# Optimization experiments

Hardware: AMD Instinct MI355X
Metric: run time of the kernel (lower is better)

The kernel has to match this reference:

```python
import jax, jax.numpy as jnp
import numpy as np

N, E, B = 20000, 320000, 64
HID, DEPTH, NFREQ = 128, 4, 8
NODE_DIM, EDGE_DIM, SG = 4, 3, 230
TWO_PI = 2.0 * np.pi


def setup_inputs() -> dict:
    key = jax.random.key(0)
    ks = jax.random.split(key, 20)
    inp = {}
    inp["x"] = jax.random.normal(ks[0], (N, NODE_DIM), jnp.float32)
    inp["edge_index"] = jax.random.randint(ks[1], (2, E), 0, N)
    inp["edge_attr"] = jax.random.normal(ks[2], (E, EDGE_DIM), jnp.float32)
    inp["batch"] = jnp.sort(jax.random.randint(ks[3], (N,), 0, B))
    inp["space_group"] = jax.random.randint(ks[4], (B,), 0, SG)
    inp["node_w"] = jax.random.normal(ks[5], (NODE_DIM, HID), jnp.float32) * 0.1
    inp["node_b"] = jnp.zeros((HID,), jnp.float32)
    inp["sg_table"] = jax.random.normal(ks[6], (SG, HID), jnp.float32) * 0.1
    inp["lin_w"] = jax.random.normal(ks[7], (DEPTH, 2 * HID + EDGE_DIM, HID), jnp.float32) * 0.05
    inp["lin_b"] = jnp.zeros((DEPTH, HID), jnp.float32)
    inp["att_w"] = jax.random.normal(ks[8], (DEPTH, 2 * HID + EDGE_DIM), jnp.float32) * 0.05
    inp["att_b"] = jnp.zeros((DEPTH,), jnp.float32)
    inp["fk_w"] = jax.random.normal(ks[9], (DEPTH, NFREQ, HID, HID), jnp.float32) * 0.1
    inp["fk_b"] = jnp.zeros((DEPTH, HID), jnp.float32)
    inp["bn_g"] = jnp.ones((DEPTH, HID), jnp.float32)
    inp["bn_b"] = jnp.zeros((DEPTH, HID), jnp.float32)
    inp["pool_w"] = jax.random.normal(ks[10], (HID,), jnp.float32) * 0.1
    inp["pool_b"] = jnp.zeros((), jnp.float32)
    inp["head_w1"] = jax.random.normal(ks[11], (4, 2 * HID, HID), jnp.float32) * 0.05
    inp["head_b1"] = jnp.zeros((4, HID), jnp.float32)
    for i, (nm, od) in enumerate([("e", 1), ("s", 3), ("c", 7), ("m", 3)]):
        inp[nm + "_w2"] = jax.random.normal(ks[12 + i], (HID, od), jnp.float32) * 0.05
        inp[nm + "_b2"] = jnp.zeros((od,), jnp.float32)
    return inp


def reference(x, edge_index, edge_attr, batch, space_group, node_w, node_b, sg_table,
              lin_w, lin_b, att_w, att_b, fk_w, fk_b, bn_g, bn_b, pool_w, pool_b,
              head_w1, head_b1, e_w2, e_b2, s_w2, s_b2, c_w2, c_b2, m_w2, m_b2):
    src, dst = edge_index[0], edge_index[1]  # x_j = x[src], x_i = x[dst]
    h = x @ node_w + node_b                  # [N, HID]
    sg = sg_table[space_group]               # [B, HID]
    freqs = jnp.arange(1, NFREQ + 1, dtype=h.dtype)
    for l in range(DEPTH):
        # edge conv: gather-concat-linear-sigmoid attention-scatter add
        tmp = jnp.concatenate([h[dst], h[src], edge_attr], axis=-1)   # [E, 2H+3]
        alpha = jax.nn.sigmoid(tmp @ att_w[l] + att_b[l])[:, None]    # [E, 1]
        msg = alpha * (tmp @ lin_w[l] + lin_b[l])                     # [E, H]
        h_conv = jax.ops.segment_sum(msg, dst, num_segments=N)
        # Fourier-Kolmogorov branch
        ang = TWO_PI * freqs[None, :, None] * h[:, None, :]           # [N, K, H]
        h_fk = (jnp.einsum('nki,kio->no', jnp.sin(ang), fk_w[l])
                + jnp.einsum('nki,kio->no', jnp.cos(ang), fk_w[l]) + fk_b[l])
        h = h_conv + h_fk
        # BatchNorm1d (batch statistics, training semantics) + ReLU; dropout = identity (eval)
        mu = h.mean(axis=0)
        var = h.var(axis=0)
        h = (h - mu) / jnp.sqrt(var + 1e-5) * bn_g[l] + bn_b[l]
        h = jax.nn.relu(h)
    # attention pool: softmax over ALL nodes (dim=0), as in the original
    a = jax.nn.softmax(h @ pool_w + pool_b, axis=0)[:, None]          # [N, 1]
    pooled = jax.ops.segment_sum(a * h, batch, num_segments=B)        # [B, H]
    comb = jnp.concatenate([pooled, sg], axis=-1)                     # [B, 2H]

    def head(i, w2, b2):
        z = jax.nn.relu(comb @ head_w1[i] + head_b1[i])
        return z @ w2 + b2

    energy = head(0, e_w2, e_b2)          # [B, 1]
    stability = head(1, s_w2, s_b2)       # [B, 3]
    crystal_system = head(2, c_w2, c_b2)  # [B, 7]
    material_type = head(3, m_w2, m_b2)   # [B, 3]
    return energy, stability, crystal_system, material_type
```

## Files before the change

kernel.cpp:

```cpp
#include <hip/hip_runtime.h>
#include <math.h>

#define HID 128
#define DEPTH 4
#define PSPLIT 16
#define SMAXB 40

typedef _Float16 half8 __attribute__((ext_vector_type(8)));
typedef float f4 __attribute__((ext_vector_type(4)));

__global__ void k_node_embed(const float* __restrict__ x, const float* __restrict__ nw,
                             const float* __restrict__ nb, float* __restrict__ h, int N) {
    int idx = blockIdx.x * blockDim.x + threadIdx.x;
    if (idx >= N * HID) return;
    int n = idx >> 7, c = idx & 127;
    float acc = nb[c];
#pragma unroll
    for (int d = 0; d < 4; ++d) acc += x[n * 4 + d] * nw[d * HID + c];
    h[idx] = acc;
}

__global__ void k_wsplit(const float* __restrict__ fkw, _Float16* __restrict__ whi,
                         _Float16* __restrict__ wlo) {
    __shared__ float sh[64][65];
    int bid = blockIdx.x;
    int l = bid >> 5; int r = bid & 31; int kb = r >> 1; int nbk = r & 1;
    const float* W = fkw + (size_t)l * 131072;
    _Float16* Hl = whi + (size_t)l * 131072;
    _Float16* Ll = wlo + (size_t)l * 131072;
    int k0 = kb * 64, n0 = nbk * 64;
    for (int i = threadIdx.x; i < 4096; i += 256) {
        int kk = i >> 6, nn = i & 63;
        sh[kk][nn] = W[(k0 + kk) * HID + n0 + nn];
    }
    __syncthreads();
    for (int i = threadIdx.x; i < 4096; i += 256) {
        int nn = i >> 6, kk = i & 63;
        float w = sh[kk][nn];
        _Float16 hi = (_Float16)w;
        _Float16 lo = (_Float16)((w - (float)hi) * 2048.f);
        Hl[(n0 + nn) * 1024 + k0 + kk] = hi;
        Ll[(n0 + nn) * 1024 + k0 + kk] = lo;
    }
}

__global__ void k_wsplit2(const float* __restrict__ linw, _Float16* __restrict__ lwhi,
                          _Float16* __restrict__ lwlo) {
    __shared__ float sh[64][65];
    int bid = blockIdx.x;
    int l = bid >> 3; int r = bid & 7; int cb = r >> 1; int kb = r & 1;
    const float* W = linw + (size_t)l * 259 * HID;
    int c0 = cb * 64, k0 = kb * 64;
    const float* base = W + (size_t)((c0 >= 128) ? 128 : 0) * HID + (c0 & 127);
    for (int i = threadIdx.x; i < 4096; i += 256) {
        int kk = i >> 6, cc = i & 63;
        sh[kk][cc] = base[(size_t)(k0 + kk) * HID + cc];
    }
    __syncthreads();
    _Float16* Hl = lwhi + (size_t)l * 32768;
    _Float16* Ll = lwlo + (size_t)l * 32768;
    for (int i = threadIdx.x; i < 4096; i += 256) {
        int cc = i >> 6, kk = i & 63;
        float w = sh[kk][cc];
        _Float16 hi = (_Float16)w;
        _Float16 lo = (_Float16)((w - (float)hi) * 2048.f);
        Hl[(size_t)(c0 + cc) * 128 + k0 + kk] = hi;
        Ll[(size_t)(c0 + cc) * 128 + k0 + kk] = lo;
    }
}

__global__ void k_hist(const int* __restrict__ dst, int* __restrict__ deg, int E) {
    int e = blockIdx.x * 256 + threadIdx.x;
    if (e < E) atomicAdd(&deg[dst[e]], 1);
}

__global__ void k_scan_a(const int* __restrict__ deg, int* __restrict__ bsum, int N) {
    __shared__ int sh[256];
    int i = blockIdx.x * 256 + threadIdx.x;
    sh[threadIdx.x] = (i < N) ? deg[i] : 0;
    __syncthreads();
    for (int off = 128; off > 0; off >>= 1) {
        if (threadIdx.x < (unsigned)off) sh[threadIdx.x] += sh[threadIdx.x + off];
        __syncthreads();
    }
    if (threadIdx.x == 0) bsum[blockIdx.x] = sh[0];
}

__global__ void k_scan_b(int* __restrict__ bsum, int nb) {
    __shared__ int sh[256];
    int v = (threadIdx.x < (unsigned)nb) ? bsum[threadIdx.x] : 0;
    sh[threadIdx.x] = v;
    __syncthreads();
    for (int off = 1; off < 256; off <<= 1) {
        int add = (threadIdx.x >= (unsigned)off) ? sh[threadIdx.x - off] : 0;
        __syncthreads();
        sh[threadIdx.x] += add;
        __syncthreads();
    }
    if (threadIdx.x < (unsigned)nb) bsum[threadIdx.x] = sh[threadIdx.x] - v;
}

__global__ void k_scan_c(const int* __restrict__ deg, const int* __restrict__ bsum,
                         int* __restrict__ offs, int* __restrict__ cursor, int N) {
    __shared__ int sh[256];
    int i = blockIdx.x * 256 + threadIdx.x;
    int v = (i < N) ? deg[i] : 0;
    sh[threadIdx.x] = v;
    __syncthreads();
    for (int off = 1; off < 256; off <<= 1) {
        int add = (threadIdx.x >= (unsigned)off) ? sh[threadIdx.x - off] : 0;
        __syncthreads();
        sh[threadIdx.x] += add;
        __syncthreads();
    }
    int ex = bsum[blockIdx.x] + sh[threadIdx.x] - v;
    if (i < N) { offs[i] = ex; cursor[i] = ex; }
    if (i == N - 1) offs[N] = ex + v;
}

__global__ void k_scatter(const int* __restrict__ src, const int* __restrict__ dst,
                          const float* __restrict__ ea, int* cursor,
                          int* __restrict__ srco, float4* __restrict__ ea3o, int E) {
    int e = blockIdx.x * 256 + threadIdx.x;
    if (e < E) {
        int d = dst[e];
        int p = atomicAdd(&cursor[d], 1);
        srco[p] = src[e];
        float4 q;
        q.x = ea[e * 3 + 0]; q.y = ea[e * 3 + 1]; q.z = ea[e * 3 + 2]; q.w = 0.f;
        ea3o[p] = q;
    }
}

__global__ void k_bstart(const int* __restrict__ batch, int* __restrict__ boffs, int N, int B) {
    int n = blockIdx.x * 256 + threadIdx.x;
    if (n >= N) return;
    int b1 = batch[n];
    if (n == 0) for (int b = 0; b <= b1; ++b) boffs[b] = 0;
    int b2 = (n + 1 < N) ? batch[n + 1] : B;
    for (int b = b1 + 1; b <= b2; ++b) boffs[b] = n + 1;
}

__global__ __launch_bounds__(512, 4) void k_nlgemm(const float* __restrict__ h,
        const _Float16* __restrict__ lwhi, const _Float16* __restrict__ lwlo,
        const float* __restrict__ linb,
        const float* __restrict__ attw, const float* __restrict__ attb,
        float* __restrict__ A1, float* __restrict__ A2,
        float* __restrict__ a1, float* __restrict__ a2, int N) {
    __shared__ _Float16 ahi[32 * 128];
    __shared__ _Float16 alo[32 * 128];
    int tid = threadIdx.x;
    int nb = blockIdx.x * 32;
    {
        int row = tid >> 4;
        int o16 = tid & 15;
        int gn = nb + row;
        int rc = (gn < N) ? gn : (N - 1);
        const float* hp = h + (size_t)rc * HID + o16 * 8;
        float hv[8];
        *(float4*)&hv[0] = *(const float4*)hp;
        *(float4*)&hv[4] = *(const float4*)(hp + 4);
        float p1 = 0.f, p2 = 0.f;
#pragma unroll
        for (int j = 0; j < 8; ++j) {
            int k = o16 * 8 + j;
            p1 += hv[j] * attw[k];
            p2 += hv[j] * attw[128 + k];
        }
        for (int off = 8; off > 0; off >>= 1) {
            p1 += __shfl_down(p1, off, 16);
            p2 += __shfl_down(p2, off, 16);
        }
        if (o16 == 0 && gn < N) {
            a1[gn] = p1 + attb[0];
            a2[gn] = p2;
        }
        int rs = row & 7;
        half8 vh, vl;
#pragma unroll
        for (int j = 0; j < 8; ++j) {
            float a = hv[j];
            _Float16 hi = (_Float16)a;
            vh[j] = hi;
            vl[j] = (_Float16)((a - (float)hi) * 2048.f);
        }
        int oct = o16 ^ rs;
        *(half8*)&ahi[row * 128 + oct * 8] = vh;
        *(half8*)&alo[row * 128 + oct * 8] = vl;
    }
    __syncthreads();
    int lane = tid & 63, wv = tid >> 6;
    int quad = lane >> 4, l16 = lane & 15;
    int n0 = wv * 32;
    f4 acc0[2][2], accL[2][2];
#pragma unroll
    for (int mi = 0; mi < 2; ++mi)
#pragma unroll
        for (int ni = 0; ni < 2; ++ni) { acc0[mi][ni] = (f4)(0.f); accL[mi][ni] = (f4)(0.f); }
    const _Float16* bhp0 = lwhi + (size_t)(n0 + l16) * 128 + quad * 8;
    const _Float16* bhp1 = lwhi + (size_t)(n0 + 16 + l16) * 128 + quad * 8;
    const _Float16* blp0 = lwlo + (size_t)(n0 + l16) * 128 + quad * 8;
    const _Float16* blp1 = lwlo + (size_t)(n0 + 16 + l16) * 128 + quad * 8;
    int rs16 = (l16 & 7) << 3;
#pragma unroll
    for (int step = 0; step < 4; ++step) {
        int ka = (step * 32 + quad * 8) ^ rs16;
        int ko = step * 32;
        half8 bh0 = *(const half8*)(bhp0 + ko);
        half8 bh1 = *(const half8*)(bhp1 + ko);
        half8 bl0 = *(const half8*)(blp0 + ko);
        half8 bl1 = *(const half8*)(blp1 + ko);
        half8 ah[2], al[2];
#pragma unroll
        for (int mi = 0; mi < 2; ++mi) {
            ah[mi] = *(const half8*)&ahi[(l16 + mi * 16) * 128 + ka];
            al[mi] = *(const half8*)&alo[(l16 + mi * 16) * 128 + ka];
        }
#pragma unroll
        for (int mi = 0; mi < 2; ++mi) {
            acc0[mi][0] = __builtin_amdgcn_mfma_f32_16x16x32_f16(ah[mi], bh0, acc0[mi][0], 0, 0, 0);
            acc0[mi][1] = __builtin_amdgcn_mfma_f32_16x16x32_f16(ah[mi], bh1, acc0[mi][1], 0, 0, 0);
            accL[mi][0] = __builtin_amdgcn_mfma_f32_16x16x32_f16(ah[mi], bl0, accL[mi][0], 0, 0, 0);
            accL[mi][1] = __builtin_amdgcn_mfma_f32_16x16x32_f16(ah[mi], bl1, accL[mi][1], 0, 0, 0);
            accL[mi][0] = __builtin_amdgcn_mfma_f32_16x16x32_f16(al[mi], bh0, accL[mi][0], 0, 0, 0);
            accL[mi][1] = __builtin_amdgcn_mfma_f32_16x16x32_f16(al[mi], bh1, accL[mi][1], 0, 0, 0);
        }
    }
    const float inv = 1.0f / 2048.0f;
#pragma unroll
    for (int mi = 0; mi < 2; ++mi)
#pragma unroll
        for (int ni = 0; ni < 2; ++ni)
#pragma unroll
            for (int r = 0; r < 4; ++r) {
                int gn = nb + mi * 16 + quad * 4 + r;
                if (gn >= N) continue;
                int cp = n0 + ni * 16 + l16;
                float val = acc0[mi][ni][r] + accL[mi][ni][r] * inv;
                if (cp < 128) A1[(size_t)gn * HID + cp] = val + linb[cp];
                else          A2[(size_t)gn * HID + cp - 128] = val;
            }
}

__global__ __launch_bounds__(256) void k_edge(const float* __restrict__ A1,
        const float* __restrict__ A2, const float* __restrict__ a1,
        const float* __restrict__ a2, const int* __restrict__ srco,
        const float4* __restrict__ ea3o, const int* __restrict__ offs,
        const float* __restrict__ linw3, const float* __restrict__ attw3,
        float* __restrict__ hconv, double* __restrict__ stats, int N) {
    __shared__ float part[8][HID + 4];
    int n = blockIdx.x;
    int tid = threadIdx.x;
    if (n == 0) stats[tid] = 0.0;
    int lane32 = tid & 31, slot = tid >> 5;
    int c4 = lane32 * 4;
    float4 w0v = *(const float4*)&linw3[c4];
    float4 w1v = *(const float4*)&linw3[HID + c4];
    float4 w2v = *(const float4*)&linw3[2 * HID + c4];
    float aw0 = attw3[0], aw1 = attw3[1], aw2 = attw3[2];
    float a1n = a1[n];
    float4 A1v = *(const float4*)&A1[(size_t)n * HID + c4];
    float4 acc; acc.x = acc.y = acc.z = acc.w = 0.f;
    int s0 = offs[n], s1 = offs[n + 1];
    for (int idx = s0 + slot; idx < s1; idx += 8) {
        int s = srco[idx];
        float4 q = ea3o[idx];
        float logit = a1n + a2[s] + q.x * aw0 + q.y * aw1 + q.z * aw2;
        float al = 1.f / (1.f + __expf(-logit));
        float4 a2v = *(const float4*)&A2[(size_t)s * HID + c4];
        float4 pre;
        pre.x = A1v.x + a2v.x + q.x * w0v.x + q.y * w1v.x + q.z * w2v.x;
        pre.y = A1v.y + a2v.y + q.x * w0v.y + q.y * w1v.y + q.z * w2v.y;
        pre.z = A1v.z + a2v.z + q.x * w0v.z + q.y * w1v.z + q.z * w2v.z;
        pre.w = A1v.w + a2v.w + q.x * w0v.w + q.y * w1v.w + q.z * w2v.w;
        acc.x += al * pre.x; acc.y += al * pre.y;
        acc.z += al * pre.z; acc.w += al * pre.w;
    }
    *(float4*)&part[slot][c4] = acc;
    __syncthreads();
    if (slot == 0) {
        float4 p = *(const float4*)&part[0][c4];
#pragma unroll
        for (int s = 1; s < 8; ++s) {
            float4 r = *(const float4*)&part[s][c4];
            p.x += r.x; p.y += r.y; p.z += r.z; p.w += r.w;
        }
        *(float4*)&hconv[(size_t)n * HID + c4] = p;
    }
}

#define FK_MT 64
__global__ __launch_bounds__(512, 4) void k_fk(const float* __restrict__ h,
        const _Float16* __restrict__ whi, const _Float16* __restrict__ wlo,
        float* __restrict__ p0, float* __restrict__ p1,
        float* __restrict__ p2, float* __restrict__ p3, int N) {
    __shared__ _Float16 ahi[FK_MT * 256];
    __shared__ _Float16 alo[FK_MT * 256];
    int tid = threadIdx.x;
    int bx = blockIdx.x;
    int nb = (bx >> 2) * FK_MT;
    int ks = bx & 3;
    int kbase = ks * 256;
    int fr0 = kbase >> 7;
    {
        int row = tid >> 3;
        int o8 = tid & 7;
        int gn = nb + row;
        int rc = (gn < N) ? gn : (N - 1);
        const float* hp = h + (size_t)rc * HID + o8 * 8;
        float hv[2][8];
        *(float4*)&hv[0][0] = *(const float4*)hp;
        *(float4*)&hv[0][4] = *(const float4*)(hp + 4);
        *(float4*)&hv[1][0] = *(const float4*)(hp + 64);
        *(float4*)&hv[1][4] = *(const float4*)(hp + 68);
        int rs = row & 7;
#pragma unroll
        for (int g = 0; g < 2; ++g) {
            float freqf = 6.2831853f * (float)(fr0 + g + 1);
#pragma unroll
            for (int s = 0; s < 2; ++s) {
                half8 vh, vl;
#pragma unroll
                for (int j = 0; j < 8; ++j) {
                    float ang = freqf * hv[s][j] + 0.78539816f;
                    float a = 1.41421356f * __sinf(ang);
                    _Float16 hi = (_Float16)a;
                    vh[j] = hi;
                    vl[j] = (_Float16)((a - (float)hi) * 2048.f);
                }
                int oct = (g * 16 + s * 8 + o8) ^ rs;
                *(half8*)&ahi[row * 256 + oct * 8] = vh;
                *(half8*)&alo[row * 256 + oct * 8] = vl;
            }
        }
    }
    __syncthreads();
    int lane = tid & 63, wv = tid >> 6;
    int quad = lane >> 4, l16 = lane & 15;
    int n0w = wv * 16;
    f4 acc0[4], accL[4];
#pragma unroll
    for (int mi = 0; mi < 4; ++mi) { acc0[mi] = (f4)(0.f); accL[mi] = (f4)(0.f); }
    const _Float16* bhp = whi + (size_t)(n0w + l16) * 1024 + kbase + quad * 8;
    const _Float16* blp = wlo + (size_t)(n0w + l16) * 1024 + kbase + quad * 8;
    int rs16 = (l16 & 7) << 3;
#pragma unroll 2
    for (int step = 0; step < 8; ++step) {
        int ka = (step * 32 + quad * 8) ^ rs16;
        int ko = step * 32;
        half8 bh = *(const half8*)(bhp + ko);
        half8 bl = *(const half8*)(blp + ko);
        half8 ah[4], al[4];
#pragma unroll
        for (int mi = 0; mi < 4; ++mi) {
            ah[mi] = *(const half8*)&ahi[(l16 + mi * 16) * 256 + ka];
            al[mi] = *(const half8*)&alo[(l16 + mi * 16) * 256 + ka];
        }
#pragma unroll
        for (int mi = 0; mi < 4; ++mi) {
            acc0[mi] = __builtin_amdgcn_mfma_f32_16x16x32_f16(ah[mi], bh, acc0[mi], 0, 0, 0);
            accL[mi] = __builtin_amdgcn_mfma_f32_16x16x32_f16(ah[mi], bl, accL[mi], 0, 0, 0);
            accL[mi] = __builtin_amdgcn_mfma_f32_16x16x32_f16(al[mi], bh, accL[mi], 0, 0, 0);
        }
    }
    float* p = (ks == 0) ? p0 : (ks == 1) ? p1 : (ks == 2) ? p2 : p3;
    const float inv = 1.0f / 2048.0f;
#pragma unroll
    for (int mi = 0; mi < 4; ++mi)
#pragma unroll
        for (int r = 0; r < 4; ++r) {
            int gn = nb + mi * 16 + quad * 4 + r;
            if (gn < N)
                p[gn * HID + n0w + l16] = acc0[mi][r] + accL[mi][r] * inv;
        }
}

__global__ __launch_bounds__(256) void k_bn_stats(float* __restrict__ hconv,
                           const float* __restrict__ p0, const float* __restrict__ p1,
                           const float* __restrict__ p2, const float* __restrict__ p3,
                           const float* __restrict__ fkb,
                           double* __restrict__ stats, int N) {
    int tid = threadIdx.x;
    int cq = tid & 31, rg = tid >> 5;
    int c4 = cq * 4;
    float4 bias = *(const float4*)&fkb[c4];
    float s1[4] = {0, 0, 0, 0}, s2[4] = {0, 0, 0, 0};
    for (int n = blockIdx.x * 8 + rg; n < N; n += gridDim.x * 8) {
        size_t idx = (size_t)n * HID + c4;
        float4 a  = *(const float4*)&hconv[idx];
        float4 b0 = *(const float4*)&p0[idx];
        float4 b1 = *(const float4*)&p1[idx];
        float4 b2 = *(const float4*)&p2[idx];
        float4 b3 = *(const float4*)&p3[idx];
        float4 v;
        v.x = a.x + b0.x + b1.x + b2.x + b3.x + bias.x;
        v.y = a.y + b0.y + b1.y + b2.y + b3.y + bias.y;
        v.z = a.z + b0.z + b1.z + b2.z + b3.z + bias.z;
        v.w = a.w + b0.w + b1.w + b2.w + b3.w + bias.w;
        *(float4*)&hconv[idx] = v;
        s1[0] += v.x; s2[0] += v.x * v.x;
        s1[1] += v.y; s2[1] += v.y * v.y;
        s1[2] += v.z; s2[2] += v.z * v.z;
        s1[3] += v.w; s2[3] += v.w * v.w;
    }
#pragma unroll
    for (int j = 0; j < 4; ++j) {
        s1[j] += __shfl_down(s1[j], 32);
        s2[j] += __shfl_down(s2[j], 32);
    }
    __shared__ float sh1[4][32][4], sh2[4][32][4];
    int wv = tid >> 6, lane = tid & 63;
    if (lane < 32) {
#pragma unroll
        for (int j = 0; j < 4; ++j) { sh1[wv][lane][j] = s1[j]; sh2[wv][lane][j] = s2[j]; }
    }
    __syncthreads();
    if (tid < 128) {
        int cq2 = tid >> 2, j2 = tid & 3;
        float t1 = sh1[0][cq2][j2] + sh1[1][cq2][j2] + sh1[2][cq2][j2] + sh1[3][cq2][j2];
        float t2 = sh2[0][cq2][j2] + sh2[1][cq2][j2] + sh2[2][cq2][j2] + sh2[3][cq2][j2];
        int c = cq2 * 4 + j2;
        atomicAdd(&stats[c], (double)t1);
        atomicAdd(&stats[128 + c], (double)t2);
    }
}

__global__ void k_bn_apply(const float* __restrict__ hsum, const double* __restrict__ stats,
                           const float* __restrict__ g, const float* __restrict__ b,
                           const float* __restrict__ pw, const float* __restrict__ pb,
                           float* __restrict__ h, float* __restrict__ s,
                           int do_score, int N) {
    int idx = blockIdx.x * 256 + threadIdx.x;
    int row = idx >> 5, cq = idx & 31;
    int c4 = cq * 4;
    int valid = row < N;
    double invN = 1.0 / (double)N;
    float p = 0.f;
    if (valid) {
        float4 hv = *(const float4*)&hsum[(size_t)row * HID + c4];
        float vin[4] = {hv.x, hv.y, hv.z, hv.w};
        float4 ov;
        float* po = &ov.x;
#pragma unroll
        for (int j = 0; j < 4; ++j) {
            int c = c4 + j;
            float mu = (float)(stats[c] * invN);
            float var = (float)(stats[128 + c] * invN) - mu * mu;
            float inv = 1.f / sqrtf(var + 1e-5f);
            float sc = g[c] * inv;
            float sh = b[c] - mu * sc;
            float oo = fmaxf(vin[j] * sc + sh, 0.f);
            po[j] = oo;
            if (do_score) p += oo * pw[c];
        }
        *(float4*)&h[(size_t)row * HID + c4] = ov;
    }
    if (do_score) {
        for (int off = 16; off > 0; off >>= 1) p += __shfl_down(p, off, 32);
        if ((threadIdx.x & 31) == 0 && valid) s[row] = p + pb[0];
    }
}

__global__ void k_smax1(const float* __restrict__ s, float* __restrict__ mzp, int N) {
    __shared__ float red[256];
    float m = -INFINITY;
    for (int n = blockIdx.x * 256 + threadIdx.x; n < N; n += SMAXB * 256)
        m = fmaxf(m, s[n]);
    red[threadIdx.x] = m;
    __syncthreads();
    for (int off = 128; off > 0; off >>= 1) {
        if (threadIdx.x < (unsigned)off)
            red[threadIdx.x] = fmaxf(red[threadIdx.x], red[threadIdx.x + off]);
        __syncthreads();
    }
    m = red[0];
    __syncthreads();
    float z = 0.f;
    for (int n = blockIdx.x * 256 + threadIdx.x; n < N; n += SMAXB * 256)
        z += __expf(s[n] - m);
    red[threadIdx.x] = z;
    __syncthreads();
    for (int off = 128; off > 0; off >>= 1) {
        if (threadIdx.x < (unsigned)off) red[threadIdx.x] += red[threadIdx.x + off];
        __syncthreads();
    }
    if (threadIdx.x == 0) { mzp[blockIdx.x * 2] = m; mzp[blockIdx.x * 2 + 1] = red[0]; }
}

__device__ __forceinline__ void combine_mz(const float* mzp, float& m, float& Z) {
    m = -INFINITY;
#pragma unroll 8
    for (int i = 0; i < SMAXB; ++i) m = fmaxf(m, mzp[i * 2]);
    Z = 0.f;
#pragma unroll 8
    for (int i = 0; i < SMAXB; ++i) Z += mzp[i * 2 + 1] * __expf(mzp[i * 2] - m);
}

__global__ void k_pool_part(const float* __restrict__ h, const float* __restrict__ s,
                            const float* __restrict__ mzp, const int* __restrict__ boffs,
                            float* __restrict__ part) {
    int b = blockIdx.x >> 4, split = blockIdx.x & (PSPLIT - 1);
    int c = threadIdx.x & 127, half = threadIdx.x >> 7;
    float m, Z;
    combine_mz(mzp, m, Z);
    (void)Z;
    int n0 = boffs[b], n1 = boffs[b + 1];
    float acc = 0.f;
    for (int n = n0 + split * 2 + half; n < n1; n += PSPLIT * 2)
        acc += __expf(s[n] - m) * h[n * HID + c];
    __shared__ float prt[2][HID];
    prt[half][c] = acc;
    __syncthreads();
    if (half == 0) part[(size_t)(b * PSPLIT + split) * HID + c] = prt[0][c] + prt[1][c];
}

__global__ void k_pool_sum(const float* __restrict__ part, const float* __restrict__ mzp,
                           float* __restrict__ pooled) {
    int b = blockIdx.x, c = threadIdx.x;
    float m, Z;
    combine_mz(mzp, m, Z);
    float acc = 0.f;
#pragma unroll
    for (int i = 0; i < PSPLIT; ++i) acc += part[(size_t)(b * PSPLIT + i) * HID + c];
    pooled[b * HID + c] = acc / Z;
}

__global__ __launch_bounds__(256) void k_head(const float* __restrict__ pooled,
                       const float* __restrict__ sg_table,
                       const int* __restrict__ space_group,
                       const float* __restrict__ hw1, const float* __restrict__ hb1,
                       const float* __restrict__ ew2, const float* __restrict__ eb2,
                       const float* __restrict__ sw2, const float* __restrict__ sb2,
                       const float* __restrict__ cw2, const float* __restrict__ cb2,
                       const float* __restrict__ mw2, const float* __restrict__ mb2,
                       float* __restrict__ out, int B) {
    __shared__ float comb[256];
    __shared__ float zred[2][128];
    __shared__ float zsh[128];
    int b = blockIdx.x >> 2, i = blockIdx.x & 3;
    int t = threadIdx.x;
    comb[t] = (t < 128) ? pooled[b * HID + t] : sg_table[space_group[b] * HID + (t - 128)];
    __syncthreads();
    int half = t >> 7, tt = t & 127;
    const float* W = hw1 + ((size_t)i * 256 + half * 128) * HID;
    const float* cb = &comb[half * 128];
    float z = 0.f;
#pragma unroll 8
    for (int k = 0; k < 128; ++k) z += cb[k] * W[k * HID + tt];
    zred[half][tt] = z;
    __syncthreads();
    if (t < 128) zsh[t] = fmaxf(zred[0][t] + zred[1][t] + hb1[i * HID + t], 0.f);
    __syncthreads();
    const int od[4] = {1, 3, 7, 3};
    const int base[4] = {0, 64, 256, 704};
    const float* w2 = (i == 0) ? ew2 : (i == 1) ? sw2 : (i == 2) ? cw2 : mw2;
    const float* b2 = (i == 0) ? eb2 : (i == 1) ? sb2 : (i == 2) ? cb2 : mb2;
    int odi = od[i];
    if (t < odi) {
        float o = b2[t];
        for (int c = 0; c < HID; ++c) o += zsh[c] * w2[c * odi + t];
        out[base[i] + b * odi + t] = o;
    }
}

extern "C" void kernel_launch(void* const* d_in, const int* in_sizes, int n_in,
                              void* d_out, int out_size, void* d_ws, size_t ws_size,
                              hipStream_t stream) {
    const float* x          = (const float*)d_in[0];
    const int*   edge_index = (const int*)d_in[1];
    const float* edge_attr  = (const float*)d_in[2];
    const int*   batch      = (const int*)d_in[3];
    const int*   space_group= (const int*)d_in[4];
    const float* node_w     = (const float*)d_in[5];
    const float* node_b     = (const float*)d_in[6];
    const float* sg_table   = (const float*)d_in[7];
    const float* lin_w      = (const float*)d_in[8];
    const float* lin_b      = (const float*)d_in[9];
    const float* att_w      = (const float*)d_in[10];
    const float* att_b      = (const float*)d_in[11];
    const float* fk_w       = (const float*)d_in[12];
    const float* fk_b       = (const float*)d_in[13];
    const float* bn_g       = (const float*)d_in[14];
    const float* bn_b       = (const float*)d_in[15];
    const float* pool_w     = (const float*)d_in[16];
    const float* pool_b     = (const float*)d_in[17];
    const float* head_w1    = (const float*)d_in[18];
    const float* head_b1    = (const float*)d_in[19];
    const float* ew2 = (const float*)d_in[20]; const float* eb2 = (const float*)d_in[21];
    const float* sw2 = (const float*)d_in[22]; const float* sb2 = (const float*)d_in[23];
    const float* cw2 = (const float*)d_in[24]; const float* cb2 = (const float*)d_in[25];
    const float* mw2 = (const float*)d_in[26]; const float* mb2 = (const float*)d_in[27];
    float* out = (float*)d_out;

    const int N = in_sizes[3];
    const int E = in_sizes[1] / 2;
    const int B = in_sizes[4];
    const int* src = edge_index;
    const int* dst = edge_index + E;

    char* w = (char*)d_ws;
    auto alloc = [&](size_t bytes) { char* p = w; w += (bytes + 255) & ~(size_t)255; return p; };
    float*  h      = (float*)alloc((size_t)N * HID * 4);
    float*  A1     = (float*)alloc((size_t)N * HID * 4);
    float*  A2     = (float*)alloc((size_t)N * HID * 4);
    float*  p2     = (float*)alloc((size_t)N * HID * 4);
    float*  p3     = (float*)alloc((size_t)N * HID * 4);
    float*  hconv  = (float*)alloc((size_t)N * HID * 4);
    float*  a1     = (float*)alloc((size_t)N * 4);
    float*  a2     = (float*)alloc((size_t)N * 4);
    float*  sbuf   = (float*)alloc((size_t)N * 4);
    int*    deg    = (int*)alloc((size_t)N * 4);
    int*    cursor = (int*)alloc((size_t)N * 4);
    int*    offs   = (int*)alloc((size_t)(N + 1) * 4);
    int*    srco   = (int*)alloc((size_t)E * 4);
    float4* ea3o   = (float4*)alloc((size_t)E * 16);
    _Float16* whi  = (_Float16*)alloc((size_t)DEPTH * 1024 * HID * 2);
    _Float16* wlo  = (_Float16*)alloc((size_t)DEPTH * 1024 * HID * 2);
    _Float16* lwhi = (_Float16*)alloc((size_t)DEPTH * 256 * HID * 2);
    _Float16* lwlo = (_Float16*)alloc((size_t)DEPTH * 256 * HID * 2);
    int*    bsum   = (int*)alloc(256 * 4);
    int*    boffs  = (int*)alloc((size_t)(B + 1) * 4);
    double* stats  = (double*)alloc(256 * 8);
    float*  mzp    = (float*)alloc(SMAXB * 2 * 4);
    float*  part   = (float*)alloc((size_t)B * PSPLIT * HID * 4);
    float*  pooled = (float*)alloc((size_t)B * HID * 4);

    const int nchunk = (N + 255) / 256;
    const int echunk = (E + 255) / 256;

    k_wsplit<<<128, 256, 0, stream>>>(fk_w, whi, wlo);
    k_wsplit2<<<32, 256, 0, stream>>>(lin_w, lwhi, lwlo);
    hipMemsetAsync(deg, 0, (size_t)N * 4, stream);
    k_hist<<<echunk, 256, 0, stream>>>(dst, deg, E);
    k_scan_a<<<nchunk, 256, 0, stream>>>(deg, bsum, N);
    k_scan_b<<<1, 256, 0, stream>>>(bsum, nchunk);
    k_scan_c<<<nchunk, 256, 0, stream>>>(deg, bsum, offs, cursor, N);
    k_scatter<<<echunk, 256, 0, stream>>>(src, dst, edge_attr, cursor, srco, ea3o, E);
    k_bstart<<<nchunk, 256, 0, stream>>>(batch, boffs, N, B);

    k_node_embed<<<(N * HID + 255) / 256, 256, 0, stream>>>(x, node_w, node_b, h, N);

    for (int l = 0; l < DEPTH; ++l) {
        const float* linw_l = lin_w + (size_t)l * 259 * HID;
        k_nlgemm<<<(N + 31) / 32, 512, 0, stream>>>(
            h, lwhi + (size_t)l * 32768, lwlo + (size_t)l * 32768,
            lin_b + l * HID, att_w + (size_t)l * 259, att_b + l,
            A1, A2, a1, a2, N);
        k_edge<<<N, 256, 0, stream>>>(A1, A2, a1, a2, srco, ea3o, offs,
                                      linw_l + 256 * HID, att_w + (size_t)l * 259 + 256,
                                      hconv, stats, N);
        k_fk<<<((N + FK_MT - 1) / FK_MT) * 4, 512, 0, stream>>>(
            h, whi + (size_t)l * 131072, wlo + (size_t)l * 131072, A1, A2, p2, p3, N);
        k_bn_stats<<<320, 256, 0, stream>>>(hconv, A1, A2, p2, p3, fk_b + l * HID, stats, N);
        k_bn_apply<<<(N * 32 + 255) / 256, 256, 0, stream>>>(
            hconv, stats, bn_g + l * HID, bn_b + l * HID, pool_w, pool_b,
            h, sbuf, (l == DEPTH - 1) ? 1 : 0, N);
    }

    k_smax1<<<SMAXB, 256, 0, stream>>>(sbuf, mzp, N);
    k_pool_part<<<B * PSPLIT, 256, 0, stream>>>(h, sbuf, mzp, boffs, part);
    k_pool_sum<<<B, 128, 0, stream>>>(part, mzp, pooled);
    k_head<<<B * 4, 256, 0, stream>>>(pooled, sg_table, space_group, head_w1, head_b1,
                                      ew2, eb2, sw2, sb2, cw2, cb2, mw2, mb2, out, B);
}
```

Baseline: 645.8 us.

## Fuse node embedding and BatchNorm apply into next layer's GEMM prologues

Removes the standalone node-embed kernel and the per-layer BN-apply kernel. The first layer's GEMM and Fourier kernels now compute the embedding from x directly, and later layers apply the previous layer's BatchNorm and ReLU while loading their input. Per-layer stats buffers are zeroed once up front, and hconv is double-buffered so the raw pre-BN activations survive until both consumers have read them. This saves one full N x HID write and read pass per layer plus launches, at the cost of recomputing the BN scale and shift in every thread of two kernels.

```diff
diff --git a/kernel.cpp b/kernel.cpp
--- a/kernel.cpp
+++ b/kernel.cpp
@@ -8,17 +8,6 @@
 
 typedef _Float16 half8 __attribute__((ext_vector_type(8)));
 typedef float f4 __attribute__((ext_vector_type(4)));
-
-__global__ void k_node_embed(const float* __restrict__ x, const float* __restrict__ nw,
-                             const float* __restrict__ nb, float* __restrict__ h, int N) {
-    int idx = blockIdx.x * blockDim.x + threadIdx.x;
-    if (idx >= N * HID) return;
-    int n = idx >> 7, c = idx & 127;
-    float acc = nb[c];
-#pragma unroll
-    for (int d = 0; d < 4; ++d) acc += x[n * 4 + d] * nw[d * HID + c];
-    h[idx] = acc;
-}
 
 __global__ void k_wsplit(const float* __restrict__ fkw, _Float16* __restrict__ whi,
                          _Float16* __restrict__ wlo) {
@@ -141,7 +130,10 @@
     for (int b = b1 + 1; b <= b2; ++b) boffs[b] = n + 1;
 }
 
-__global__ __launch_bounds__(512, 4) void k_nlgemm(const float* __restrict__ h,
+__global__ __launch_bounds__(512, 4) void k_nlgemm(const float* __restrict__ hsrc,
+        const float* __restrict__ x, const float* __restrict__ nw, const float* __restrict__ nbv,
+        const double* __restrict__ bnst, const float* __restrict__ bng, const float* __restrict__ bnb,
+        int mode,
         const _Float16* __restrict__ lwhi, const _Float16* __restrict__ lwlo,
         const float* __restrict__ linb,
         const float* __restrict__ attw, const float* __restrict__ attb,
@@ -156,10 +148,31 @@
         int o16 = tid & 15;
         int gn = nb + row;
         int rc = (gn < N) ? gn : (N - 1);
-        const float* hp = h + (size_t)rc * HID + o16 * 8;
         float hv[8];
-        *(float4*)&hv[0] = *(const float4*)hp;
-        *(float4*)&hv[4] = *(const float4*)(hp + 4);
+        if (mode == 0) {
+            float4 xr = *(const float4*)&x[(size_t)rc * 4];
+#pragma unroll
+            for (int j = 0; j < 8; ++j) {
+                int c = o16 * 8 + j;
+                hv[j] = nbv[c] + xr.x * nw[c] + xr.y * nw[HID + c]
+                       + xr.z * nw[2 * HID + c] + xr.w * nw[3 * HID + c];
+            }
+        } else {
+            const float* hp = hsrc + (size_t)rc * HID + o16 * 8;
+            *(float4*)&hv[0] = *(const float4*)hp;
+            *(float4*)&hv[4] = *(const float4*)(hp + 4);
+            double invN = 1.0 / (double)N;
+#pragma unroll
+            for (int j = 0; j < 8; ++j) {
+                int c = o16 * 8 + j;
+                float mu = (float)(bnst[c] * invN);
+                float var = (float)(bnst[128 + c] * invN) - mu * mu;
+                float inv = 1.f / sqrtf(var + 1e-5f);
+                float sc = bng[c] * inv;
+                float sh = bnb[c] - mu * sc;
+                hv[j] = fmaxf(hv[j] * sc + sh, 0.f);
+            }
+        }
         float p1 = 0.f, p2 = 0.f;
 #pragma unroll
         for (int j = 0; j < 8; ++j) {
@@ -247,11 +260,10 @@
         const float* __restrict__ a2, const int* __restrict__ srco,
         const float4* __restrict__ ea3o, const int* __restrict__ offs,
         const float* __restrict__ linw3, const float* __restrict__ attw3,
-        float* __restrict__ hconv, double* __restrict__ stats, int N) {
+        float* __restrict__ hconv, int N) {
     __shared__ float part[8][HID + 4];
     int n = blockIdx.x;
     int tid = threadIdx.x;
-    if (n == 0) stats[tid] = 0.0;
     int lane32 = tid & 31, slot = tid >> 5;
     int c4 = lane32 * 4;
     float4 w0v = *(const float4*)&linw3[c4];
@@ -290,7 +302,10 @@
 }
 
 #define FK_MT 64
-__global__ __launch_bounds__(512, 4) void k_fk(const float* __restrict__ h,
+__global__ __launch_bounds__(512, 4) void k_fk(const float* __restrict__ hsrc,
+        const float* __restrict__ x, const float* __restrict__ nw, const float* __restrict__ nbv,
+        const double* __restrict__ bnst, const float* __restrict__ bng, const float* __restrict__ bnb,
+        int mode,
         const _Float16* __restrict__ whi, const _Float16* __restrict__ wlo,
         float* __restrict__ p0, float* __restrict__ p1,
         float* __restrict__ p2, float* __restrict__ p3, int N) {
@@ -307,12 +322,37 @@
         int o8 = tid & 7;
         int gn = nb + row;
         int rc = (gn < N) ? gn : (N - 1);
-        const float* hp = h + (size_t)rc * HID + o8 * 8;
         float hv[2][8];
-        *(float4*)&hv[0][0] = *(const float4*)hp;
-        *(float4*)&hv[0][4] = *(const float4*)(hp + 4);
-        *(float4*)&hv[1][0] = *(const float4*)(hp + 64);
-        *(float4*)&hv[1][4] = *(const float4*)(hp + 68);
+        if (mode == 0) {
+            float4 xr = *(const float4*)&x[(size_t)rc * 4];
+#pragma unroll
+            for (int s = 0; s < 2; ++s)
+#pragma unroll
+                for (int j = 0; j < 8; ++j) {
+                    int c = s * 64 + o8 * 8 + j;
+                    hv[s][j] = nbv[c] + xr.x * nw[c] + xr.y * nw[HID + c]
+                              + xr.z * nw[2 * HID + c] + xr.w * nw[3 * HID + c];
+                }
+        } else {
+            const float* hp = hsrc + (size_t)rc * HID + o8 * 8;
+            *(float4*)&hv[0][0] = *(const float4*)hp;
+            *(float4*)&hv[0][4] = *(const float4*)(hp + 4);
+            *(float4*)&hv[1][0] = *(const float4*)(hp + 64);
+            *(float4*)&hv[1][4] = *(const float4*)(hp + 68);
+            double invN = 1.0 / (double)N;
+#pragma unroll
+            for (int s = 0; s < 2; ++s)
+#pragma unroll
+                for (int j = 0; j < 8; ++j) {
+                    int c = s * 64 + o8 * 8 + j;
+                    float mu = (float)(bnst[c] * invN);
+                    float var = (float)(bnst[128 + c] * invN) - mu * mu;
+                    float inv = 1.f / sqrtf(var + 1e-5f);
+                    float sc = bng[c] * inv;
+                    float sh = bnb[c] - mu * sc;
+                    hv[s][j] = fmaxf(hv[s][j] * sc + sh, 0.f);
+                }
+        }
         int rs = row & 7;
 #pragma unroll
         for (int g = 0; g < 2; ++g) {
@@ -605,7 +645,8 @@
     float*  A2     = (float*)alloc((size_t)N * HID * 4);
     float*  p2     = (float*)alloc((size_t)N * HID * 4);
     float*  p3     = (float*)alloc((size_t)N * HID * 4);
-    float*  hconv  = (float*)alloc((size_t)N * HID * 4);
+    float*  hcv0   = (float*)alloc((size_t)N * HID * 4);
+    float*  hcv1   = (float*)alloc((size_t)N * HID * 4);
     float*  a1     = (float*)alloc((size_t)N * 4);
     float*  a2     = (float*)alloc((size_t)N * 4);
     float*  sbuf   = (float*)alloc((size_t)N * 4);
@@ -620,7 +661,7 @@
     _Float16* lwlo = (_Float16*)alloc((size_t)DEPTH * 256 * HID * 2);
     int*    bsum   = (int*)alloc(256 * 4);
     int*    boffs  = (int*)alloc((size_t)(B + 1) * 4);
-    double* stats  = (double*)alloc(256 * 8);
+    double* stats  = (double*)alloc((size_t)DEPTH * 256 * 8);
     float*  mzp    = (float*)alloc(SMAXB * 2 * 4);
     float*  part   = (float*)alloc((size_t)B * PSPLIT * HID * 4);
     float*  pooled = (float*)alloc((size_t)B * HID * 4);
@@ -631,6 +672,7 @@
     k_wsplit<<<128, 256, 0, stream>>>(fk_w, whi, wlo);
     k_wsplit2<<<32, 256, 0, stream>>>(lin_w, lwhi, lwlo);
     hipMemsetAsync(deg, 0, (size_t)N * 4, stream);
+    hipMemsetAsync(stats, 0, (size_t)DEPTH * 256 * 8, stream);
     k_hist<<<echunk, 256, 0, stream>>>(dst, deg, E);
     k_scan_a<<<nchunk, 256, 0, stream>>>(deg, bsum, N);
     k_scan_b<<<1, 256, 0, stream>>>(bsum, nchunk);
@@ -638,24 +680,33 @@
     k_scatter<<<echunk, 256, 0, stream>>>(src, dst, edge_attr, cursor, srco, ea3o, E);
     k_bstart<<<nchunk, 256, 0, stream>>>(batch, boffs, N, B);
 
-    k_node_embed<<<(N * HID + 255) / 256, 256, 0, stream>>>(x, node_w, node_b, h, N);
-
+    float* hcv[2] = {hcv0, hcv1};
     for (int l = 0; l < DEPTH; ++l) {
         const float* linw_l = lin_w + (size_t)l * 259 * HID;
+        int mode = (l == 0) ? 0 : 1;
+        const double* bst = (l == 0) ? (const double*)nullptr : stats + (size_t)(l - 1) * 256;
+        const float* bgl = bn_g + (size_t)((l == 0) ? 0 : (l - 1)) * HID;
+        const float* bbl = bn_b + (size_t)((l == 0) ? 0 : (l - 1)) * HID;
+        const float* hprev = (l == 0) ? h : hcv[(l - 1) & 1];
+        float* hcur = hcv[l & 1];
         k_nlgemm<<<(N + 31) / 32, 512, 0, stream>>>(
-            h, lwhi + (size_t)l * 32768, lwlo + (size_t)l * 32768,
+            hprev, x, node_w, node_b, bst, bgl, bbl, mode,
+            lwhi + (size_t)l * 32768, lwlo + (size_t)l * 32768,
             lin_b + l * HID, att_w + (size_t)l * 259, att_b + l,
             A1, A2, a1, a2, N);
         k_edge<<<N, 256, 0, stream>>>(A1, A2, a1, a2, srco, ea3o, offs,
                                       linw_l + 256 * HID, att_w + (size_t)l * 259 + 256,
-                                      hconv, stats, N);
+                                      hcur, N);
         k_fk<<<((N + FK_MT - 1) / FK_MT) * 4, 512, 0, stream>>>(
-            h, whi + (size_t)l * 131072, wlo + (size_t)l * 131072, A1, A2, p2, p3, N);
-        k_bn_stats<<<320, 256, 0, stream>>>(hconv, A1, A2, p2, p3, fk_b + l * HID, stats, N);
-        k_bn_apply<<<(N * 32 + 255) / 256, 256, 0, stream>>>(
-            hconv, stats, bn_g + l * HID, bn_b + l * HID, pool_w, pool_b,
-            h, sbuf, (l == DEPTH - 1) ? 1 : 0, N);
-    }
+            hprev, x, node_w, node_b, bst, bgl, bbl, mode,
+            whi + (size_t)l * 131072, wlo + (size_t)l * 131072, A1, A2, p2, p3, N);
+        k_bn_stats<<<320, 256, 0, stream>>>(hcur, A1, A2, p2, p3, fk_b + l * HID,
+                                            stats + (size_t)l * 256, N);
+    }
+    k_bn_apply<<<(N * 32 + 255) / 256, 256, 0, stream>>>(
+        hcv[(DEPTH - 1) & 1], stats + (size_t)(DEPTH - 1) * 256,
+        bn_g + (size_t)(DEPTH - 1) * HID, bn_b + (size_t)(DEPTH - 1) * HID,
+        pool_w, pool_b, h, sbuf, 1, N);
 
     k_smax1<<<SMAXB, 256, 0, stream>>>(sbuf, mzp, N);
     k_pool_part<<<B * PSPLIT, 256, 0, stream>>>(h, sbuf, mzp, boffs, part);
```

After: 677.1 us. 1.05x slower.
